# Kernel optimization log

Measured on AMD Instinct MI355X. Metric: run time of the kernel, lower is better.

## Reference

```python
import jax, jax.numpy as jnp
import numpy as np

N = 50000   # num entities
E = 300000  # num edges
H = 256     # hidden_dim
TD = 768    # text_emb_dim
R = 200     # num_relations (decoder)
R2 = 400    # conv relations (2*R)
NB = 8      # num_bases
T = 8192    # num triples scored
LN_EPS = 1e-5


def setup_inputs() -> dict:
    key = jax.random.key(0)
    ks = jax.random.split(key, 20)
    rn = lambda i, shape, s=0.05: jax.random.normal(ks[i], shape, dtype=jnp.float32) * s
    return {
        "ent_emb": rn(0, (N, H)),
        "text_base": rn(1, (N, TD)),
        "text_proj_w": rn(2, (H, TD)),
        "text_proj_b": jnp.zeros((H,), jnp.float32),
        "ln_g": jnp.ones((H,), jnp.float32),
        "ln_b": jnp.zeros((H,), jnp.float32),
        "comp1": rn(3, (R2, NB), 0.2),
        "basis1": rn(4, (NB, H, H)),
        "root1": rn(5, (H, H)),
        "bias1": jnp.zeros((H,), jnp.float32),
        "comp2": rn(6, (R2, NB), 0.2),
        "basis2": rn(7, (NB, H, H)),
        "root2": rn(8, (H, H)),
        "bias2": jnp.zeros((H,), jnp.float32),
        "rel_emb": rn(9, (R, H)),
        "edge_src": jax.random.randint(ks[10], (E,), 0, N),
        "edge_dst": jax.random.randint(ks[11], (E,), 0, N),
        "edge_type": jax.random.randint(ks[12], (E,), 0, R2),
        "heads": jax.random.randint(ks[13], (T,), 0, N),
        "rels": jax.random.randint(ks[14], (T,), 0, R),
        "tails": jax.random.randint(ks[15], (T,), 0, N),
    }


def layer_norm(x, g, b):
    mu = jnp.mean(x, axis=-1, keepdims=True)
    var = jnp.mean(jnp.square(x - mu), axis=-1, keepdims=True)
    return g * (x - mu) * jax.lax.rsqrt(var + LN_EPS) + b


def rgcn_conv(x, comp, basis, root, bias, src, dst, etype):
    # Basis-decomposed RGCN: W_r = sum_b comp[r,b] * basis[b]
    # message e: x[src_e] @ W_{etype_e}; scatter-add to dst with in-degree norm.
    deg = jax.ops.segment_sum(jnp.ones((E,), x.dtype), dst, num_segments=N)
    inv_deg = 1.0 / jnp.maximum(deg, 1.0)                 # [N]
    xb = jnp.einsum('nd,bdf->nbf', x, basis)              # [N, NB, H]
    c = comp[etype]                                       # [E, NB]
    msg = jnp.zeros((E, x.shape[-1]), x.dtype)
    for b in range(NB):  # small fixed basis loop avoids [E,NB,H] intermediate
        msg = msg + c[:, b:b + 1] * xb[:, b, :][src]
    agg = jax.ops.segment_sum(msg, dst, num_segments=N) * inv_deg[:, None]
    return agg + x @ root + bias


def reference(ent_emb, text_base, text_proj_w, text_proj_b, ln_g, ln_b,
              comp1, basis1, root1, bias1, comp2, basis2, root2, bias2,
              rel_emb, edge_src, edge_dst, edge_type, heads, rels, tails):
    # base entity features: embedding + projected text, then LayerNorm
    x = ent_emb + text_base @ text_proj_w.T + text_proj_b
    x = layer_norm(x, ln_g, ln_b)
    # two RGCN layers with ReLU (eval mode: dropout = identity)
    x = jax.nn.relu(rgcn_conv(x, comp1, basis1, root1, bias1, edge_src, edge_dst, edge_type))
    x = jax.nn.relu(rgcn_conv(x, comp2, basis2, root2, bias2, edge_src, edge_dst, edge_type))
    # ComplEx decoder: split hidden into real/imag halves
    h, t, r = x[heads], x[tails], rel_emb[rels]
    d2 = H // 2
    hr, hi = h[:, :d2], h[:, d2:]
    tr, ti = t[:, :d2], t[:, d2:]
    rr, ri = r[:, :d2], r[:, d2:]
    score = jnp.sum(hr * rr * tr + hi * rr * ti + hr * ri * ti - hi * ri * tr, axis=-1)
    return score
```

## Files before the change

kernel.cpp:

```cpp
#include <hip/hip_runtime.h>
#include <hip/hip_bf16.h>

#define NN  50000
#define EE  300000
#define HH  256
#define TDD 768
#define NBB 8
#define TTT 8192

typedef __bf16 bf16x8 __attribute__((ext_vector_type(8)));
typedef float  f32x4  __attribute__((ext_vector_type(4)));

__device__ __forceinline__ float b2f(unsigned short u) {
    union { unsigned int i; float f; } v; v.i = (unsigned int)u << 16; return v.f;
}
__device__ __forceinline__ unsigned short f2b(float f) {
    union { float f; unsigned int i; } v; v.f = f;
    unsigned int r = (v.i + 0x7fffu + ((v.i >> 16) & 1u)) >> 16;
    return (unsigned short)r;
}
__device__ __forceinline__ void gload16(const void* g, void* l) {
    __builtin_amdgcn_global_load_lds(
        (const __attribute__((address_space(1))) void*)g,
        (__attribute__((address_space(3))) void*)l, 16, 0, 0);
}

template<int EPI>
__global__ __launch_bounds__(256) void gemm16_k(
    const unsigned short* __restrict__ A1, int lda1,
    const unsigned short* __restrict__ A2, int lda2, int KS,
    const unsigned short* __restrict__ Bt, int K,
    unsigned short* __restrict__ C, int M,
    const float* __restrict__ add, const float* __restrict__ bias)
{
    __shared__ unsigned short As[4096];
    __shared__ unsigned short Bs[4096];
    const int tid  = threadIdx.x;
    const int lane = tid & 63;
    const int wid  = tid >> 6;
    const int bm   = blockIdx.x * 128;
    const int bn   = blockIdx.y * 128;
    const int lrow = lane & 15;
    const int lk   = lane >> 4;
    const int wm   = (wid & 1) * 64;
    const int wn   = (wid >> 1) * 64;

    f32x4 acc[4][4];
#pragma unroll
    for (int i = 0; i < 4; ++i)
#pragma unroll
        for (int j = 0; j < 4; ++j) acc[i][j] = (f32x4){0.f, 0.f, 0.f, 0.f};

    for (int k0 = 0; k0 < K; k0 += 32) {
        const unsigned short* Ap; int lda, kb;
        if (k0 < KS) { Ap = A1; lda = lda1; kb = k0; }
        else         { Ap = A2; lda = lda2; kb = k0 - KS; }
#pragma unroll
        for (int p = 0; p < 2; ++p) {
            int cbar = p * 4 + wid;
            int s  = cbar * 64 + lane;
            int cg = s >> 7, r = s & 127;
            int gm = bm + r; if (gm >= M) gm = M - 1;
            gload16(Ap + (size_t)gm * lda + kb + cg * 8, &As[cbar * 512]);
            gload16(Bt + (size_t)(bn + r) * K + k0 + cg * 8, &Bs[cbar * 512]);
        }
        __syncthreads();

        bf16x8 af[4], bfr[4];
#pragma unroll
        for (int i = 0; i < 4; ++i) {
            af[i]  = *(const bf16x8*)&As[lk * 1024 + (wm + i * 16 + lrow) * 8];
            bfr[i] = *(const bf16x8*)&Bs[lk * 1024 + (wn + i * 16 + lrow) * 8];
        }
#pragma unroll
        for (int i = 0; i < 4; ++i)
#pragma unroll
            for (int j = 0; j < 4; ++j)
                acc[i][j] = __builtin_amdgcn_mfma_f32_16x16x32_bf16(
                    af[i], bfr[j], acc[i][j], 0, 0, 0);
        __syncthreads();
    }

#pragma unroll
    for (int i = 0; i < 4; ++i) {
        int row0 = bm + wm + i * 16 + lk * 4;
#pragma unroll
        for (int j = 0; j < 4; ++j) {
            int col = bn + wn + j * 16 + lrow;
            float bb = bias[col];
            f32x4 v = acc[i][j];
#pragma unroll
            for (int e = 0; e < 4; ++e) {
                int gm = row0 + e;
                if (gm < M) {
                    float o = v[e] + bb;
                    if (EPI == 1) o += add[(size_t)gm * HH + col];
                    if (EPI == 2) o = fmaxf(o, 0.f);
                    C[(size_t)gm * HH + col] = f2b(o);
                }
            }
        }
    }
}

__global__ void cast4_k(const float* __restrict__ in, unsigned short* __restrict__ out,
                        int n4)
{
    int i = blockIdx.x * blockDim.x + threadIdx.x;
    if (i >= n4) return;
    float4 v = *(const float4*)(in + (size_t)i * 4);
    ushort4 o;
    o.x = f2b(v.x); o.y = f2b(v.y); o.z = f2b(v.z); o.w = f2b(v.w);
    *(ushort4*)(out + (size_t)i * 4) = o;
}

__global__ __launch_bounds__(256) void tcast_k(
    const float* __restrict__ basis1, const float* __restrict__ root1,
    const float* __restrict__ basis2, const float* __restrict__ root2,
    unsigned short* __restrict__ Bt1, unsigned short* __restrict__ Bt2)
{
    __shared__ float Ls[64][68];
    int z = blockIdx.z;
    int layer = z / 9, m = z % 9;
    const float* src = layer ? (m < 8 ? basis2 + m * 65536 : root2)
                             : (m < 8 ? basis1 + m * 65536 : root1);
    unsigned short* dst = layer ? Bt2 : Bt1;
    int coloff = (m < 8) ? m * 256 : 2048;
    int ft = blockIdx.x * 64, dt = blockIdx.y * 64;
    int tid = threadIdx.x;
    int rr = tid >> 4, c4 = (tid & 15) << 2;
#pragma unroll
    for (int p = 0; p < 4; ++p) {
        int dl = p * 16 + rr;
        float4 v = *(const float4*)(src + (size_t)(dt + dl) * HH + ft + c4);
        Ls[c4 + 0][dl] = v.x; Ls[c4 + 1][dl] = v.y;
        Ls[c4 + 2][dl] = v.z; Ls[c4 + 3][dl] = v.w;
    }
    __syncthreads();
#pragma unroll
    for (int q = 0; q < 4; ++q) {
        int fl = q * 16 + rr;
        ushort4 o;
        o.x = f2b(Ls[fl][c4 + 0]); o.y = f2b(Ls[fl][c4 + 1]);
        o.z = f2b(Ls[fl][c4 + 2]); o.w = f2b(Ls[fl][c4 + 3]);
        *(ushort4*)(dst + (size_t)(ft + fl) * 2304 + coloff + dt + c4) = o;
    }
}

__global__ __launch_bounds__(256) void ln_k(
    const unsigned short* __restrict__ in, unsigned short* __restrict__ out,
    const float* __restrict__ g, const float* __restrict__ b)
{
    int row  = blockIdx.x * 4 + (threadIdx.x >> 6);
    int lane = threadIdx.x & 63;
    if (row >= NN) return;
    ushort4 u = *(const ushort4*)(in + (size_t)row * HH + lane * 4);
    float x0 = b2f(u.x), x1 = b2f(u.y), x2 = b2f(u.z), x3 = b2f(u.w);
    float s = x0 + x1 + x2 + x3;
#pragma unroll
    for (int o = 1; o < 64; o <<= 1) s += __shfl_xor(s, o);
    float mu = s * (1.0f / HH);
    float d0 = x0 - mu, d1 = x1 - mu, d2 = x2 - mu, d3 = x3 - mu;
    float q = d0 * d0 + d1 * d1 + d2 * d2 + d3 * d3;
#pragma unroll
    for (int o = 1; o < 64; o <<= 1) q += __shfl_xor(q, o);
    float rstd = rsqrtf(q * (1.0f / HH) + 1e-5f);
    int c = lane * 4;
    ushort4 o4;
    o4.x = f2b(g[c + 0] * d0 * rstd + b[c + 0]);
    o4.y = f2b(g[c + 1] * d1 * rstd + b[c + 1]);
    o4.z = f2b(g[c + 2] * d2 * rstd + b[c + 2]);
    o4.w = f2b(g[c + 3] * d3 * rstd + b[c + 3]);
    *(ushort4*)(out + (size_t)row * HH + c) = o4;
}

__global__ void hist_k(const int* __restrict__ dst, int* __restrict__ cnt)
{
    int i = blockIdx.x * blockDim.x + threadIdx.x;
    if (i < EE) atomicAdd(&cnt[dst[i]], 1);
}

__global__ void scan_blk_k(const int* __restrict__ cnt, int* __restrict__ rp,
                           int* __restrict__ bsum)
{
    __shared__ int s[256];
    int tid = threadIdx.x;
    int d = blockIdx.x * 256 + tid;
    int v = (d < NN) ? cnt[d] : 0;
    s[tid] = v;
    __syncthreads();
#pragma unroll
    for (int o = 1; o < 256; o <<= 1) {
        int t = (tid >= o) ? s[tid - o] : 0;
        __syncthreads();
        s[tid] += t;
        __syncthreads();
    }
    if (d < NN) rp[d] = s[tid] - v;
    if (tid == 255) bsum[blockIdx.x] = s[255];
}

__global__ void scan_top_k(int* __restrict__ bsum, int* __restrict__ boff, int nb)
{
    __shared__ int s[256];
    int tid = threadIdx.x;
    int v = (tid < nb) ? bsum[tid] : 0;
    s[tid] = v;
    __syncthreads();
#pragma unroll
    for (int o = 1; o < 256; o <<= 1) {
        int t = (tid >= o) ? s[tid - o] : 0;
        __syncthreads();
        s[tid] += t;
        __syncthreads();
    }
    if (tid < nb) boff[tid] = s[tid] - v;
}

__global__ void scan_add_k(int* __restrict__ rp, const int* __restrict__ boff,
                           int* __restrict__ cur, const int* __restrict__ cnt,
                           float* __restrict__ invdeg)
{
    int d = blockIdx.x * blockDim.x + threadIdx.x;
    if (d < NN) {
        int r = rp[d] + boff[d >> 8];
        rp[d] = r;
        cur[d] = r;
        invdeg[d] = 1.0f / fmaxf((float)cnt[d], 1.0f);
    }
    if (d == 0) rp[NN] = EE;
}

__global__ void scatter_k(const int* __restrict__ src, const int* __restrict__ dst,
                          const int* __restrict__ et, int* __restrict__ cur,
                          int* __restrict__ csr_src, int* __restrict__ csr_et)
{
    int e = blockIdx.x * blockDim.x + threadIdx.x;
    if (e >= EE) return;
    int p = atomicAdd(&cur[dst[e]], 1);
    csr_src[p] = src[e];
    csr_et[p]  = et[e];
}

__global__ __launch_bounds__(256) void agg_k(
    const unsigned short* __restrict__ x, const float* __restrict__ comp,
    const int* __restrict__ rp, const int* __restrict__ csr_src,
    const int* __restrict__ csr_et, const float* __restrict__ invdeg,
    unsigned short* __restrict__ y)
{
    int d = blockIdx.x * 4 + (threadIdx.x >> 6);
    if (d >= NN) return;
    int lane = threadIdx.x & 63;
    int beg = rp[d], end = rp[d + 1];

    float4 acc[NBB];
#pragma unroll
    for (int b = 0; b < NBB; ++b) acc[b] = make_float4(0.f, 0.f, 0.f, 0.f);

    for (int e = beg; e < end; ++e) {
        int s = csr_src[e];
        int t = csr_et[e];
        float4 c0 = *(const float4*)(comp + (size_t)t * NBB);
        float4 c1 = *(const float4*)(comp + (size_t)t * NBB + 4);
        ushort4 u = *(const ushort4*)(x + (size_t)s * HH + lane * 4);
        float xv0 = b2f(u.x), xv1 = b2f(u.y), xv2 = b2f(u.z), xv3 = b2f(u.w);
        float cc[NBB] = {c0.x, c0.y, c0.z, c0.w, c1.x, c1.y, c1.z, c1.w};
#pragma unroll
        for (int b = 0; b < NBB; ++b) {
            acc[b].x = fmaf(cc[b], xv0, acc[b].x);
            acc[b].y = fmaf(cc[b], xv1, acc[b].y);
            acc[b].z = fmaf(cc[b], xv2, acc[b].z);
            acc[b].w = fmaf(cc[b], xv3, acc[b].w);
        }
    }
    float sc = invdeg[d];
    unsigned short* yp = y + (size_t)d * (NBB * HH) + lane * 4;
#pragma unroll
    for (int b = 0; b < NBB; ++b) {
        ushort4 o;
        o.x = f2b(acc[b].x * sc); o.y = f2b(acc[b].y * sc);
        o.z = f2b(acc[b].z * sc); o.w = f2b(acc[b].w * sc);
        *(ushort4*)(yp + (size_t)b * HH) = o;
    }
}

__global__ __launch_bounds__(256) void score_k(
    const unsigned short* __restrict__ x, const float* __restrict__ rel,
    const int* __restrict__ heads, const int* __restrict__ rels,
    const int* __restrict__ tails, float* __restrict__ out)
{
    int i = blockIdx.x * 4 + (threadIdx.x >> 6);
    if (i >= TTT) return;
    int lane = threadIdx.x & 63;
    const unsigned short* h = x + (size_t)heads[i] * HH;
    const unsigned short* t = x + (size_t)tails[i] * HH;
    const float*          r = rel + (size_t)rels[i] * HH;
    int j = lane * 2;
    ushort2 hru = *(const ushort2*)(h + j), hiu = *(const ushort2*)(h + 128 + j);
    ushort2 tru = *(const ushort2*)(t + j), tiu = *(const ushort2*)(t + 128 + j);
    float2 rr = *(const float2*)(r + j), ri = *(const float2*)(r + 128 + j);
    float hr0 = b2f(hru.x), hr1 = b2f(hru.y), hi0 = b2f(hiu.x), hi1 = b2f(hiu.y);
    float tr0 = b2f(tru.x), tr1 = b2f(tru.y), ti0 = b2f(tiu.x), ti1 = b2f(tiu.y);
    float acc = hr0 * rr.x * tr0 + hi0 * rr.x * ti0
              + hr0 * ri.x * ti0 - hi0 * ri.x * tr0
              + hr1 * rr.y * tr1 + hi1 * rr.y * ti1
              + hr1 * ri.y * ti1 - hi1 * ri.y * tr1;
#pragma unroll
    for (int o = 1; o < 64; o <<= 1) acc += __shfl_xor(acc, o);
    if (lane == 0) out[i] = acc;
}

extern "C" void kernel_launch(void* const* d_in, const int* in_sizes, int n_in,
                              void* d_out, int out_size, void* d_ws, size_t ws_size,
                              hipStream_t stream)
{
    const float* ent_emb     = (const float*)d_in[0];
    const float* text_base   = (const float*)d_in[1];
    const float* text_proj_w = (const float*)d_in[2];
    const float* text_proj_b = (const float*)d_in[3];
    const float* ln_g        = (const float*)d_in[4];
    const float* ln_b        = (const float*)d_in[5];
    const float* comp1       = (const float*)d_in[6];
    const float* basis1      = (const float*)d_in[7];
    const float* root1       = (const float*)d_in[8];
    const float* bias1       = (const float*)d_in[9];
    const float* comp2       = (const float*)d_in[10];
    const float* basis2      = (const float*)d_in[11];
    const float* root2       = (const float*)d_in[12];
    const float* bias2       = (const float*)d_in[13];
    const float* rel_emb     = (const float*)d_in[14];
    const int*   edge_src    = (const int*)d_in[15];
    const int*   edge_dst    = (const int*)d_in[16];
    const int*   edge_type   = (const int*)d_in[17];
    const int*   heads       = (const int*)d_in[18];
    const int*   rels        = (const int*)d_in[19];
    const int*   tails       = (const int*)d_in[20];
    float* out = (float*)d_out;

    char* ws = (char*)d_ws;
    size_t off = 0;
    auto carve = [&](size_t bytes) -> void* {
        void* p = ws + off;
        off = (off + bytes + 255) & ~(size_t)255;
        return p;
    };
    unsigned short* x0b  = (unsigned short*)carve((size_t)NN * HH * 2);
    unsigned short* x1b  = (unsigned short*)carve((size_t)NN * HH * 2);
    unsigned short* y16  = (unsigned short*)carve((size_t)NN * NBB * HH * 2);
    unsigned short* tb16 = (unsigned short*)carve((size_t)NN * TDD * 2);
    unsigned short* W16  = (unsigned short*)carve((size_t)HH * TDD * 2);
    unsigned short* Bt1  = (unsigned short*)carve((size_t)HH * 2304 * 2);
    unsigned short* Bt2  = (unsigned short*)carve((size_t)HH * 2304 * 2);
    int*   cnt     = (int*)  carve((size_t)NN * 4);
    int*   rp      = (int*)  carve((size_t)(NN + 1) * 4);
    int*   cur     = (int*)  carve((size_t)NN * 4);
    float* invdeg  = (float*)carve((size_t)NN * 4);
    int*   csr_src = (int*)  carve((size_t)EE * 4);
    int*   csr_et  = (int*)  carve((size_t)EE * 4);
    int*   bsum    = (int*)  carve(256 * 4);
    int*   boff    = (int*)  carve(256 * 4);

    const dim3 blk(256);
    const int NBLK = (NN + 255) / 256;
    const dim3 gemm_grid((NN + 127) / 128, 2);

    hipMemsetAsync(cnt, 0, (size_t)NN * 4, stream);
    hist_k<<<(EE + 255) / 256, blk, 0, stream>>>(edge_dst, cnt);
    scan_blk_k<<<NBLK, blk, 0, stream>>>(cnt, rp, bsum);
    scan_top_k<<<1, blk, 0, stream>>>(bsum, boff, NBLK);
    scan_add_k<<<NBLK, blk, 0, stream>>>(rp, boff, cur, cnt, invdeg);
    scatter_k<<<(EE + 255) / 256, blk, 0, stream>>>(
        edge_src, edge_dst, edge_type, cur, csr_src, csr_et);

    cast4_k<<<(NN * TDD / 4 + 255) / 256, blk, 0, stream>>>(text_base, tb16, NN * TDD / 4);
    cast4_k<<<(HH * TDD / 4 + 255) / 256, blk, 0, stream>>>(text_proj_w, W16, HH * TDD / 4);
    tcast_k<<<dim3(4, 4, 18), blk, 0, stream>>>(basis1, root1, basis2, root2, Bt1, Bt2);

    gemm16_k<1><<<gemm_grid, blk, 0, stream>>>(
        tb16, TDD, tb16, TDD, TDD, W16, TDD, x1b, NN, ent_emb, text_proj_b);
    ln_k<<<(NN + 3) / 4, blk, 0, stream>>>(x1b, x0b, ln_g, ln_b);

    for (int layer = 0; layer < 2; ++layer) {
        const unsigned short* xin  = layer ? x1b : x0b;
        unsigned short*       xout = layer ? x0b : x1b;
        const unsigned short* Bt   = layer ? Bt2 : Bt1;
        const float*          comp = layer ? comp2 : comp1;
        const float*          bias = layer ? bias2 : bias1;

        agg_k<<<(NN + 3) / 4, blk, 0, stream>>>(
            xin, comp, rp, csr_src, csr_et, invdeg, y16);

        gemm16_k<2><<<gemm_grid, blk, 0, stream>>>(
            y16, NBB * HH, xin, HH, NBB * HH, Bt, NBB * HH + HH,
            xout, NN, nullptr, bias);
    }

    score_k<<<(TTT + 3) / 4, blk, 0, stream>>>(x0b, rel_emb, heads, rels, tails, out);
}
```

Measured before the change: 1.024 ms.

## Fuse text cast and LayerNorm into GEMM with full-width double-buffered tiles

Removes the separate fp32-to-bf16 cast of text_base and the standalone LayerNorm kernel. The first GEMM now reads fp32 text_base directly and converts it in registers. Its epilogue adds ent_emb and the bias, then computes per-row LayerNorm using cross-wave shared-memory reductions. The GEMM tile changes to 64 rows by the full 256 columns with double-buffered LDS prefetch, so each A tile is read once per row block. In exchange, variance is computed as E[x^2]-mu^2, B reloads per block grow, and LDS use rises.

```diff
diff --git a/kernel.cpp b/kernel.cpp
--- a/kernel.cpp
+++ b/kernel.cpp
@@ -10,6 +10,7 @@
 
 typedef __bf16 bf16x8 __attribute__((ext_vector_type(8)));
 typedef float  f32x4  __attribute__((ext_vector_type(4)));
+typedef unsigned short u16x8 __attribute__((ext_vector_type(8)));
 
 __device__ __forceinline__ float b2f(unsigned short u) {
     union { unsigned int i; float f; } v; v.i = (unsigned int)u << 16; return v.f;
@@ -25,25 +26,27 @@
         (__attribute__((address_space(3))) void*)l, 16, 0, 0);
 }
 
-template<int EPI>
+template<int EPI, int ADT>
 __global__ __launch_bounds__(256) void gemm16_k(
-    const unsigned short* __restrict__ A1, int lda1,
-    const unsigned short* __restrict__ A2, int lda2, int KS,
+    const void* __restrict__ A1v, int lda1,
+    const void* __restrict__ A2v, int lda2, int KS,
     const unsigned short* __restrict__ Bt, int K,
     unsigned short* __restrict__ C, int M,
-    const float* __restrict__ add, const float* __restrict__ bias)
-{
-    __shared__ unsigned short As[4096];
-    __shared__ unsigned short Bs[4096];
+    const float* __restrict__ add, const float* __restrict__ bias,
+    const float* __restrict__ lng, const float* __restrict__ lnb)
+{
+    __shared__ unsigned short As[2][2048];
+    __shared__ unsigned short Bs[2][8192];
+    __shared__ float lredS[64][4];
+    __shared__ float lredQ[64][4];
     const int tid  = threadIdx.x;
     const int lane = tid & 63;
     const int wid  = tid >> 6;
-    const int bm   = blockIdx.x * 128;
-    const int bn   = blockIdx.y * 128;
+    const int bm   = blockIdx.x * 64;
     const int lrow = lane & 15;
     const int lk   = lane >> 4;
-    const int wm   = (wid & 1) * 64;
-    const int wn   = (wid >> 1) * 64;
+    const int wn   = wid * 64;
+    const int NT   = K / 32;
 
     f32x4 acc[4][4];
 #pragma unroll
@@ -51,26 +54,42 @@
 #pragma unroll
         for (int j = 0; j < 4; ++j) acc[i][j] = (f32x4){0.f, 0.f, 0.f, 0.f};
 
-    for (int k0 = 0; k0 < K; k0 += 32) {
+    auto stageB = [&](int half, int k0) {
+#pragma unroll
+        for (int p = 0; p < 4; ++p) {
+            int q  = p * 4 + wid;
+            int cg = q >> 2;
+            int r  = (q & 3) * 64 + lane;
+            gload16(Bt + (size_t)r * K + k0 + cg * 8, &Bs[half][q * 512]);
+        }
+    };
+    auto stageA0 = [&](int half, int k0) {
         const unsigned short* Ap; int lda, kb;
-        if (k0 < KS) { Ap = A1; lda = lda1; kb = k0; }
-        else         { Ap = A2; lda = lda2; kb = k0 - KS; }
-#pragma unroll
-        for (int p = 0; p < 2; ++p) {
-            int cbar = p * 4 + wid;
-            int s  = cbar * 64 + lane;
-            int cg = s >> 7, r = s & 127;
-            int gm = bm + r; if (gm >= M) gm = M - 1;
-            gload16(Ap + (size_t)gm * lda + kb + cg * 8, &As[cbar * 512]);
-            gload16(Bt + (size_t)(bn + r) * K + k0 + cg * 8, &Bs[cbar * 512]);
-        }
-        __syncthreads();
-
+        if (k0 < KS) { Ap = (const unsigned short*)A1v; lda = lda1; kb = k0; }
+        else         { Ap = (const unsigned short*)A2v; lda = lda2; kb = k0 - KS; }
+        int gm = bm + lane; if (gm >= M) gm = M - 1;
+        gload16(Ap + (size_t)gm * lda + kb + wid * 8, &As[half][wid * 512]);
+    };
+    auto loadA1 = [&](int k0, float4& u0, float4& u1) {
+        const float* Ap = (const float*)A1v;
+        int cg = tid >> 6, r = tid & 63;
+        int gm = bm + r; if (gm >= M) gm = M - 1;
+        const float* p = Ap + (size_t)gm * lda1 + k0 + cg * 8;
+        u0 = *(const float4*)p;
+        u1 = *(const float4*)(p + 4);
+    };
+    auto writeA1 = [&](int half, float4 u0, float4 u1) {
+        u16x8 o;
+        o[0] = f2b(u0.x); o[1] = f2b(u0.y); o[2] = f2b(u0.z); o[3] = f2b(u0.w);
+        o[4] = f2b(u1.x); o[5] = f2b(u1.y); o[6] = f2b(u1.z); o[7] = f2b(u1.w);
+        *(u16x8*)&As[half][tid * 8] = o;
+    };
+    auto compute = [&](int half) {
         bf16x8 af[4], bfr[4];
 #pragma unroll
         for (int i = 0; i < 4; ++i) {
-            af[i]  = *(const bf16x8*)&As[lk * 1024 + (wm + i * 16 + lrow) * 8];
-            bfr[i] = *(const bf16x8*)&Bs[lk * 1024 + (wn + i * 16 + lrow) * 8];
+            af[i]  = *(const bf16x8*)&As[half][(lk * 64  + i * 16 + lrow) * 8];
+            bfr[i] = *(const bf16x8*)&Bs[half][(lk * 256 + wn + i * 16 + lrow) * 8];
         }
 #pragma unroll
         for (int i = 0; i < 4; ++i)
@@ -78,28 +97,116 @@
             for (int j = 0; j < 4; ++j)
                 acc[i][j] = __builtin_amdgcn_mfma_f32_16x16x32_bf16(
                     af[i], bfr[j], acc[i][j], 0, 0, 0);
-        __syncthreads();
-    }
-
-#pragma unroll
-    for (int i = 0; i < 4; ++i) {
-        int row0 = bm + wm + i * 16 + lk * 4;
-#pragma unroll
-        for (int j = 0; j < 4; ++j) {
-            int col = bn + wn + j * 16 + lrow;
-            float bb = bias[col];
-            f32x4 v = acc[i][j];
-#pragma unroll
-            for (int e = 0; e < 4; ++e) {
-                int gm = row0 + e;
-                if (gm < M) {
-                    float o = v[e] + bb;
-                    if (EPI == 1) o += add[(size_t)gm * HH + col];
-                    if (EPI == 2) o = fmaxf(o, 0.f);
-                    C[(size_t)gm * HH + col] = f2b(o);
+    };
+
+    if (ADT == 0) {
+        stageA0(0, 0);
+    } else {
+        float4 a0, a1;
+        loadA1(0, a0, a1);
+        writeA1(0, a0, a1);
+    }
+    stageB(0, 0);
+
+    int cur = 0;
+    for (int t = 0; t < NT; ++t) {
+        __syncthreads();
+        const bool pf = (t + 1 < NT);
+        float4 pa0, pa1;
+        if (pf) {
+            if (ADT == 0) stageA0(cur ^ 1, (t + 1) * 32);
+            else          loadA1((t + 1) * 32, pa0, pa1);
+            stageB(cur ^ 1, (t + 1) * 32);
+        }
+        compute(cur);
+        if (pf && ADT == 1) writeA1(cur ^ 1, pa0, pa1);
+        cur ^= 1;
+    }
+
+    if (EPI == 2) {
+#pragma unroll
+        for (int i = 0; i < 4; ++i) {
+#pragma unroll
+            for (int j = 0; j < 4; ++j) {
+                int col = wn + j * 16 + lrow;
+                float bb = bias[col];
+                f32x4 v = acc[i][j];
+#pragma unroll
+                for (int e = 0; e < 4; ++e) {
+                    int gm = bm + i * 16 + lk * 4 + e;
+                    if (gm < M)
+                        C[(size_t)gm * HH + col] = f2b(fmaxf(v[e] + bb, 0.f));
                 }
             }
         }
+    } else {
+        float sum_[4][4] = {};
+        float sq_[4][4]  = {};
+#pragma unroll
+        for (int i = 0; i < 4; ++i)
+#pragma unroll
+            for (int j = 0; j < 4; ++j) {
+                int col = wn + j * 16 + lrow;
+                float tb = bias[col];
+#pragma unroll
+                for (int e = 0; e < 4; ++e) {
+                    int gm = bm + i * 16 + lk * 4 + e;
+                    if (gm >= M) gm = M - 1;
+                    float o = acc[i][j][e] + add[(size_t)gm * HH + col] + tb;
+                    acc[i][j][e] = o;
+                    sum_[i][e] += o;
+                    sq_[i][e]  += o * o;
+                }
+            }
+#pragma unroll
+        for (int m = 1; m < 16; m <<= 1)
+#pragma unroll
+            for (int i = 0; i < 4; ++i)
+#pragma unroll
+                for (int e = 0; e < 4; ++e) {
+                    sum_[i][e] += __shfl_xor(sum_[i][e], m);
+                    sq_[i][e]  += __shfl_xor(sq_[i][e],  m);
+                }
+        if (lrow == 0) {
+#pragma unroll
+            for (int i = 0; i < 4; ++i)
+#pragma unroll
+                for (int e = 0; e < 4; ++e) {
+                    int rl = i * 16 + lk * 4 + e;
+                    lredS[rl][wid] = sum_[i][e];
+                    lredQ[rl][wid] = sq_[i][e];
+                }
+        }
+        __syncthreads();
+        float mus[4][4], rstds[4][4];
+#pragma unroll
+        for (int i = 0; i < 4; ++i)
+#pragma unroll
+            for (int e = 0; e < 4; ++e) {
+                int rl = i * 16 + lk * 4 + e;
+                float4 s4 = *(const float4*)lredS[rl];
+                float4 q4 = *(const float4*)lredQ[rl];
+                float mu = (s4.x + s4.y + s4.z + s4.w) * (1.0f / HH);
+                float mq = (q4.x + q4.y + q4.z + q4.w) * (1.0f / HH);
+                float var = mq - mu * mu;
+                mus[i][e]   = mu;
+                rstds[i][e] = rsqrtf(var + 1e-5f);
+            }
+#pragma unroll
+        for (int i = 0; i < 4; ++i)
+#pragma unroll
+            for (int j = 0; j < 4; ++j) {
+                int col = wn + j * 16 + lrow;
+                float gg = lng[col], bb = lnb[col];
+#pragma unroll
+                for (int e = 0; e < 4; ++e) {
+                    int gm = bm + i * 16 + lk * 4 + e;
+                    if (gm < M) {
+                        float o = gg * (acc[i][j][e] - mus[i][e]) * rstds[i][e] + bb;
+                        C[(size_t)gm * HH + col] = f2b(o);
+                    }
+                }
+            }
     }
 }
 
@@ -145,33 +252,6 @@
         o.z = f2b(Ls[fl][c4 + 2]); o.w = f2b(Ls[fl][c4 + 3]);
         *(ushort4*)(dst + (size_t)(ft + fl) * 2304 + coloff + dt + c4) = o;
     }
-}
-
-__global__ __launch_bounds__(256) void ln_k(
-    const unsigned short* __restrict__ in, unsigned short* __restrict__ out,
-    const float* __restrict__ g, const float* __restrict__ b)
-{
-    int row  = blockIdx.x * 4 + (threadIdx.x >> 6);
-    int lane = threadIdx.x & 63;
-    if (row >= NN) return;
-    ushort4 u = *(const ushort4*)(in + (size_t)row * HH + lane * 4);
-    float x0 = b2f(u.x), x1 = b2f(u.y), x2 = b2f(u.z), x3 = b2f(u.w);
-    float s = x0 + x1 + x2 + x3;
-#pragma unroll
-    for (int o = 1; o < 64; o <<= 1) s += __shfl_xor(s, o);
-    float mu = s * (1.0f / HH);
-    float d0 = x0 - mu, d1 = x1 - mu, d2 = x2 - mu, d3 = x3 - mu;
-    float q = d0 * d0 + d1 * d1 + d2 * d2 + d3 * d3;
-#pragma unroll
-    for (int o = 1; o < 64; o <<= 1) q += __shfl_xor(q, o);
-    float rstd = rsqrtf(q * (1.0f / HH) + 1e-5f);
-    int c = lane * 4;
-    ushort4 o4;
-    o4.x = f2b(g[c + 0] * d0 * rstd + b[c + 0]);
-    o4.y = f2b(g[c + 1] * d1 * rstd + b[c + 1]);
-    o4.z = f2b(g[c + 2] * d2 * rstd + b[c + 2]);
-    o4.w = f2b(g[c + 3] * d3 * rstd + b[c + 3]);
-    *(ushort4*)(out + (size_t)row * HH + c) = o4;
 }
 
 __global__ void hist_k(const int* __restrict__ dst, int* __restrict__ cnt)
@@ -347,7 +427,6 @@
     unsigned short* x0b  = (unsigned short*)carve((size_t)NN * HH * 2);
     unsigned short* x1b  = (unsigned short*)carve((size_t)NN * HH * 2);
     unsigned short* y16  = (unsigned short*)carve((size_t)NN * NBB * HH * 2);
-    unsigned short* tb16 = (unsigned short*)carve((size_t)NN * TDD * 2);
     unsigned short* W16  = (unsigned short*)carve((size_t)HH * TDD * 2);
     unsigned short* Bt1  = (unsigned short*)carve((size_t)HH * 2304 * 2);
     unsigned short* Bt2  = (unsigned short*)carve((size_t)HH * 2304 * 2);
@@ -362,7 +441,7 @@
 
     const dim3 blk(256);
     const int NBLK = (NN + 255) / 256;
-    const dim3 gemm_grid((NN + 127) / 128, 2);
+    const int GG = (NN + 63) / 64;
 
     hipMemsetAsync(cnt, 0, (size_t)NN * 4, stream);
     hist_k<<<(EE + 255) / 256, blk, 0, stream>>>(edge_dst, cnt);
@@ -372,13 +451,12 @@
     scatter_k<<<(EE + 255) / 256, blk, 0, stream>>>(
         edge_src, edge_dst, edge_type, cur, csr_src, csr_et);
 
-    cast4_k<<<(NN * TDD / 4 + 255) / 256, blk, 0, stream>>>(text_base, tb16, NN * TDD / 4);
     cast4_k<<<(HH * TDD / 4 + 255) / 256, blk, 0, stream>>>(text_proj_w, W16, HH * TDD / 4);
     tcast_k<<<dim3(4, 4, 18), blk, 0, stream>>>(basis1, root1, basis2, root2, Bt1, Bt2);
 
-    gemm16_k<1><<<gemm_grid, blk, 0, stream>>>(
-        tb16, TDD, tb16, TDD, TDD, W16, TDD, x1b, NN, ent_emb, text_proj_b);
-    ln_k<<<(NN + 3) / 4, blk, 0, stream>>>(x1b, x0b, ln_g, ln_b);
+    gemm16_k<3, 1><<<GG, blk, 0, stream>>>(
+        text_base, TDD, text_base, TDD, TDD, W16, TDD,
+        x0b, NN, ent_emb, text_proj_b, ln_g, ln_b);
 
     for (int layer = 0; layer < 2; ++layer) {
         const unsigned short* xin  = layer ? x1b : x0b;
@@ -390,9 +468,9 @@
         agg_k<<<(NN + 3) / 4, blk, 0, stream>>>(
             xin, comp, rp, csr_src, csr_et, invdeg, y16);
 
-        gemm16_k<2><<<gemm_grid, blk, 0, stream>>>(
+        gemm16_k<2, 0><<<GG, blk, 0, stream>>>(
             y16, NBB * HH, xin, HH, NBB * HH, Bt, NBB * HH + HH,
-            xout, NN, nullptr, bias);
+            xout, NN, nullptr, bias, nullptr, nullptr);
     }
 
     score_k<<<(TTT + 3) / 4, blk, 0, stream>>>(x0b, rel_emb, heads, rels, tails, out);
```

New measurement: 1.118 ms. 1.09x slower.
